# Kernel optimization log

Hardware: AMD Instinct MI355X
Metric: run time of the kernel (lower is better)

## Reference

```python
import jax, jax.numpy as jnp
import numpy as np

NUM_GRAPHS = 256  # B: number of graphs in the ragged batch
EMBED = 256       # input_dim / MHA embed_dim
N_NODES = 200000


def setup_inputs() -> dict:
    key = jax.random.key(0)
    k1, k2, k3, k4, k5, k6 = jax.random.split(key, 6)
    x = jax.random.normal(k1, (N_NODES, EMBED), dtype=jnp.float32)
    in_proj_w = jax.random.normal(k2, (3 * EMBED, EMBED), dtype=jnp.float32) * 0.02
    in_proj_b = jax.random.normal(k3, (3 * EMBED,), dtype=jnp.float32) * 0.02
    out_proj_w = jax.random.normal(k4, (EMBED, EMBED), dtype=jnp.float32) * 0.02
    out_proj_b = jax.random.normal(k5, (EMBED,), dtype=jnp.float32) * 0.02
    batch = jnp.sort(jax.random.randint(k6, (N_NODES,), 0, NUM_GRAPHS)).astype(jnp.int64)
    return {"x": x, "in_proj_w": in_proj_w, "in_proj_b": in_proj_b,
            "out_proj_w": out_proj_w, "out_proj_b": out_proj_b, "batch": batch}


def reference(x, in_proj_w, in_proj_b, out_proj_w, out_proj_b, batch):
    E = x.shape[1]
    # global_mean_pool: per-graph mean of node features -> [B, E]
    sums = jax.ops.segment_sum(x, batch, num_segments=NUM_GRAPHS)
    counts = jax.ops.segment_sum(jnp.ones((x.shape[0],), x.dtype), batch,
                                 num_segments=NUM_GRAPHS)
    g = sums / jnp.maximum(counts, 1.0)[:, None]  # [B, E]
    # MultiheadAttention with a single K/V vector per graph: softmax over S=1
    # is identically 1, so attention output = out_proj(V_proj(g)) for every
    # query node of that graph (Q path contributes nothing).
    Wv = in_proj_w[2 * E:3 * E]
    bv = in_proj_b[2 * E:3 * E]
    v = g @ Wv.T + bv                       # [B, E] value projection
    out_graph = v @ out_proj_w.T + out_proj_b  # [B, E] output projection
    # broadcast back to nodes (torch.cat over per-graph slices)
    return out_graph[batch]                 # [N, E]
```

## Files before the change

### kernel.cpp

```cpp
#include <hip/hip_runtime.h>

#define EMBED   256
#define NGRAPH  256
#define NW      8
#define BLOCK   (NW * 64)

__global__ __launch_bounds__(BLOCK, 1) void fused_kernel(
    const float* __restrict__ x, const int* __restrict__ batch,
    const float* __restrict__ in_w, const float* __restrict__ in_b,
    const float* __restrict__ out_w, const float* __restrict__ out_b,
    float* __restrict__ out, int nNodes) {
  const int g = blockIdx.x;
  const int t = threadIdx.x;
  const int q  = t >> 6;
  const int c4 = t & 63;

  int n0, n1;
  { int a = 0, b = nNodes;
    while (a < b) { int m = (a + b) >> 1; (batch[m] < g) ? (a = m + 1) : (b = m); }
    n0 = a; }
  { int a = n0, b = nNodes;
    while (a < b) { int m = (a + b) >> 1; (batch[m] <= g) ? (a = m + 1) : (b = m); }
    n1 = a; }
  const int cnt = n1 - n0;

  const float4* xp = (const float4*)x + (size_t)n0 * (EMBED / 4) + c4;
  float4 a0 = make_float4(0.f, 0.f, 0.f, 0.f);
  float4 a1 = make_float4(0.f, 0.f, 0.f, 0.f);
  int i = q;
  for (; i + 7 * NW < cnt; i += 8 * NW) {
    float4 v0 = xp[(size_t)(i         ) * (EMBED / 4)];
    float4 v1 = xp[(size_t)(i + 1 * NW) * (EMBED / 4)];
    float4 v2 = xp[(size_t)(i + 2 * NW) * (EMBED / 4)];
    float4 v3 = xp[(size_t)(i + 3 * NW) * (EMBED / 4)];
    float4 v4 = xp[(size_t)(i + 4 * NW) * (EMBED / 4)];
    float4 v5 = xp[(size_t)(i + 5 * NW) * (EMBED / 4)];
    float4 v6 = xp[(size_t)(i + 6 * NW) * (EMBED / 4)];
    float4 v7 = xp[(size_t)(i + 7 * NW) * (EMBED / 4)];
    a0.x += v0.x + v1.x; a0.y += v0.y + v1.y; a0.z += v0.z + v1.z; a0.w += v0.w + v1.w;
    a1.x += v2.x + v3.x; a1.y += v2.y + v3.y; a1.z += v2.z + v3.z; a1.w += v2.w + v3.w;
    a0.x += v4.x + v5.x; a0.y += v4.y + v5.y; a0.z += v4.z + v5.z; a0.w += v4.w + v5.w;
    a1.x += v6.x + v7.x; a1.y += v6.y + v7.y; a1.z += v6.z + v7.z; a1.w += v6.w + v7.w;
  }
  for (; i < cnt; i += NW) {
    float4 v = xp[(size_t)i * (EMBED / 4)];
    a0.x += v.x; a0.y += v.y; a0.z += v.z; a0.w += v.w;
  }
  a0.x += a1.x; a0.y += a1.y; a0.z += a1.z; a0.w += a1.w;

  __shared__ float4 red4[NW][EMBED / 4];
  __shared__ float sg[EMBED];
  __shared__ float sv[EMBED];
  __shared__ float so[EMBED];
  red4[q][c4] = a0;
  __syncthreads();

  const float inv = 1.0f / fmaxf((float)cnt, 1.0f);
  if (t < EMBED) {
    const float* rf = (const float*)red4;
    float s = 0.f;
#pragma unroll
    for (int k = 0; k < NW; ++k) s += rf[k * EMBED + t];
    sg[t] = s * inv;
  }
  __syncthreads();

  if (t < EMBED) {
    float acc = in_b[2 * EMBED + t];
    const float4* wrow = (const float4*)(in_w + (size_t)(2 * EMBED + t) * EMBED);
#pragma unroll 8
    for (int k4 = 0; k4 < EMBED / 4; ++k4) {
      const float4 w = wrow[k4];
      const int k = k4 * 4;
      acc += sg[k] * w.x + sg[k + 1] * w.y + sg[k + 2] * w.z + sg[k + 3] * w.w;
    }
    sv[t] = acc;
  }
  __syncthreads();

  if (t < EMBED) {
    float acc = out_b[t];
    const float4* wrow = (const float4*)(out_w + (size_t)t * EMBED);
#pragma unroll 8
    for (int k4 = 0; k4 < EMBED / 4; ++k4) {
      const float4 w = wrow[k4];
      const int k = k4 * 4;
      acc += sv[k] * w.x + sv[k + 1] * w.y + sv[k + 2] * w.z + sv[k + 3] * w.w;
    }
    so[t] = acc;
  }
  __syncthreads();

  const float4 oval = ((const float4*)so)[c4];
  float4* op = (float4*)out + c4;
  int n = n0 + q;
  for (; n + 3 * NW < n1; n += 4 * NW) {
    op[(size_t)(n         ) * (EMBED / 4)] = oval;
    op[(size_t)(n + 1 * NW) * (EMBED / 4)] = oval;
    op[(size_t)(n + 2 * NW) * (EMBED / 4)] = oval;
    op[(size_t)(n + 3 * NW) * (EMBED / 4)] = oval;
  }
  for (; n < n1; n += NW) {
    op[(size_t)n * (EMBED / 4)] = oval;
  }
}

extern "C" void kernel_launch(void* const* d_in, const int* in_sizes, int n_in,
                              void* d_out, int out_size, void* d_ws, size_t ws_size,
                              hipStream_t stream) {
  const float* x     = (const float*)d_in[0];
  const float* in_w  = (const float*)d_in[1];
  const float* in_b  = (const float*)d_in[2];
  const float* out_w = (const float*)d_in[3];
  const float* out_b = (const float*)d_in[4];
  const int*   batch = (const int*)d_in[5];
  const int nNodes = in_sizes[5];

  fused_kernel<<<NGRAPH, BLOCK, 0, stream>>>(x, batch, in_w, in_b, out_w, out_b,
                                             (float*)d_out, nNodes);
}
```

Measured before the change: 374.8 us.

## Split fused kernel into partial-sum, per-graph projection, and grid-wide broadcast kernels

The single per-graph kernel becomes three. The first splits each graph's node reduction across four blocks and writes partial sums. The second combines the partials and runs the two matvecs per graph. The third broadcasts rows to all nodes with a grid-stride loop, a batch lookup per element and nontemporal stores. The aim is better occupancy and load balance than 256 blocks with one block per CU, where the reduction and the output writes of each graph were serialized. In exchange it adds two kernel launches, round trips through the workspace, and an extra batch read per output float4. If the workspace is too small, partials fall back to being stored in the output buffer.

```diff
diff --git a/kernel.cpp b/kernel.cpp
--- a/kernel.cpp
+++ b/kernel.cpp
@@ -2,16 +2,21 @@
 
 #define EMBED   256
 #define NGRAPH  256
-#define NW      8
-#define BLOCK   (NW * 64)
+#define P       4
+#define BLOCK1  512
+#define NW1     (BLOCK1 / 64)
+#define WPG     (P * NW1)
+#define BLOCK3  256
+#define NB3     2048
 
-__global__ __launch_bounds__(BLOCK, 1) void fused_kernel(
+typedef float f32x4 __attribute__((ext_vector_type(4)));
+
+__global__ __launch_bounds__(BLOCK1, 8) void seg_partial(
     const float* __restrict__ x, const int* __restrict__ batch,
-    const float* __restrict__ in_w, const float* __restrict__ in_b,
-    const float* __restrict__ out_w, const float* __restrict__ out_b,
-    float* __restrict__ out, int nNodes) {
-  const int g = blockIdx.x;
-  const int t = threadIdx.x;
+    float* __restrict__ partial, int nNodes) {
+  const int g  = blockIdx.x >> 2;
+  const int p  = blockIdx.x & (P - 1);
+  const int t  = threadIdx.x;
   const int q  = t >> 6;
   const int c4 = t & 63;
 
@@ -25,83 +30,114 @@
   const int cnt = n1 - n0;
 
   const float4* xp = (const float4*)x + (size_t)n0 * (EMBED / 4) + c4;
+  const int w = p * NW1 + q;
   float4 a0 = make_float4(0.f, 0.f, 0.f, 0.f);
   float4 a1 = make_float4(0.f, 0.f, 0.f, 0.f);
-  int i = q;
-  for (; i + 7 * NW < cnt; i += 8 * NW) {
-    float4 v0 = xp[(size_t)(i         ) * (EMBED / 4)];
-    float4 v1 = xp[(size_t)(i + 1 * NW) * (EMBED / 4)];
-    float4 v2 = xp[(size_t)(i + 2 * NW) * (EMBED / 4)];
-    float4 v3 = xp[(size_t)(i + 3 * NW) * (EMBED / 4)];
-    float4 v4 = xp[(size_t)(i + 4 * NW) * (EMBED / 4)];
-    float4 v5 = xp[(size_t)(i + 5 * NW) * (EMBED / 4)];
-    float4 v6 = xp[(size_t)(i + 6 * NW) * (EMBED / 4)];
-    float4 v7 = xp[(size_t)(i + 7 * NW) * (EMBED / 4)];
+  int i = w;
+  for (; i + 7 * WPG < cnt; i += 8 * WPG) {
+    float4 v0 = xp[(size_t)(i          ) * (EMBED / 4)];
+    float4 v1 = xp[(size_t)(i + 1 * WPG) * (EMBED / 4)];
+    float4 v2 = xp[(size_t)(i + 2 * WPG) * (EMBED / 4)];
+    float4 v3 = xp[(size_t)(i + 3 * WPG) * (EMBED / 4)];
+    float4 v4 = xp[(size_t)(i + 4 * WPG) * (EMBED / 4)];
+    float4 v5 = xp[(size_t)(i + 5 * WPG) * (EMBED / 4)];
+    float4 v6 = xp[(size_t)(i + 6 * WPG) * (EMBED / 4)];
+    float4 v7 = xp[(size_t)(i + 7 * WPG) * (EMBED / 4)];
     a0.x += v0.x + v1.x; a0.y += v0.y + v1.y; a0.z += v0.z + v1.z; a0.w += v0.w + v1.w;
     a1.x += v2.x + v3.x; a1.y += v2.y + v3.y; a1.z += v2.z + v3.z; a1.w += v2.w + v3.w;
     a0.x += v4.x + v5.x; a0.y += v4.y + v5.y; a0.z += v4.z + v5.z; a0.w += v4.w + v5.w;
     a1.x += v6.x + v7.x; a1.y += v6.y + v7.y; a1.z += v6.z + v7.z; a1.w += v6.w + v7.w;
   }
-  for (; i < cnt; i += NW) {
+  for (; i < cnt; i += WPG) {
     float4 v = xp[(size_t)i * (EMBED / 4)];
     a0.x += v.x; a0.y += v.y; a0.z += v.z; a0.w += v.w;
   }
   a0.x += a1.x; a0.y += a1.y; a0.z += a1.z; a0.w += a1.w;
 
-  __shared__ float4 red4[NW][EMBED / 4];
-  __shared__ float sg[EMBED];
-  __shared__ float sv[EMBED];
-  __shared__ float so[EMBED];
+  __shared__ float4 red4[NW1][EMBED / 4];
   red4[q][c4] = a0;
   __syncthreads();
-
-  const float inv = 1.0f / fmaxf((float)cnt, 1.0f);
   if (t < EMBED) {
     const float* rf = (const float*)red4;
     float s = 0.f;
 #pragma unroll
-    for (int k = 0; k < NW; ++k) s += rf[k * EMBED + t];
-    sg[t] = s * inv;
+    for (int k = 0; k < NW1; ++k) s += rf[k * EMBED + t];
+    partial[((size_t)p * NGRAPH + g) * EMBED + t] = s;
   }
+}
+
+__global__ __launch_bounds__(EMBED, 1) void graph_rows(
+    const float* __restrict__ partial, const int* __restrict__ batch,
+    const float* __restrict__ in_w, const float* __restrict__ in_b,
+    const float* __restrict__ out_w, const float* __restrict__ out_b,
+    float* __restrict__ rows, int nNodes) {
+  const int g = blockIdx.x;
+  const int t = threadIdx.x;
+
+  int n0, n1;
+  { int a = 0, b = nNodes;
+    while (a < b) { int m = (a + b) >> 1; (batch[m] < g) ? (a = m + 1) : (b = m); }
+    n0 = a; }
+  { int a = n0, b = nNodes;
+    while (a < b) { int m = (a + b) >> 1; (batch[m] <= g) ? (a = m + 1) : (b = m); }
+    n1 = a; }
+  const float inv = 1.0f / fmaxf((float)(n1 - n0), 1.0f);
+
+  __shared__ float sg[EMBED];
+  __shared__ float sv[EMBED];
+
+  float s = 0.f;
+#pragma unroll
+  for (int p = 0; p < P; ++p) s += partial[((size_t)p * NGRAPH + g) * EMBED + t];
+  sg[t] = s * inv;
   __syncthreads();
 
-  if (t < EMBED) {
-    float acc = in_b[2 * EMBED + t];
-    const float4* wrow = (const float4*)(in_w + (size_t)(2 * EMBED + t) * EMBED);
+  float acc = in_b[2 * EMBED + t];
+  const float4* wrow = (const float4*)(in_w + (size_t)(2 * EMBED + t) * EMBED);
 #pragma unroll 8
-    for (int k4 = 0; k4 < EMBED / 4; ++k4) {
-      const float4 w = wrow[k4];
-      const int k = k4 * 4;
-      acc += sg[k] * w.x + sg[k + 1] * w.y + sg[k + 2] * w.z + sg[k + 3] * w.w;
-    }
-    sv[t] = acc;
+  for (int k4 = 0; k4 < EMBED / 4; ++k4) {
+    const float4 w = wrow[k4];
+    const int k = k4 * 4;
+    acc += sg[k] * w.x + sg[k + 1] * w.y + sg[k + 2] * w.z + sg[k + 3] * w.w;
   }
+  sv[t] = acc;
   __syncthreads();
 
-  if (t < EMBED) {
-    float acc = out_b[t];
-    const float4* wrow = (const float4*)(out_w + (size_t)t * EMBED);
+  float acc2 = out_b[t];
+  const float4* wrow2 = (const float4*)(out_w + (size_t)t * EMBED);
 #pragma unroll 8
-    for (int k4 = 0; k4 < EMBED / 4; ++k4) {
-      const float4 w = wrow[k4];
-      const int k = k4 * 4;
-      acc += sv[k] * w.x + sv[k + 1] * w.y + sv[k + 2] * w.z + sv[k + 3] * w.w;
-    }
-    so[t] = acc;
+  for (int k4 = 0; k4 < EMBED / 4; ++k4) {
+    const float4 w = wrow2[k4];
+    const int k = k4 * 4;
+    acc2 += sv[k] * w.x + sv[k + 1] * w.y + sv[k + 2] * w.z + sv[k + 3] * w.w;
   }
-  __syncthreads();
+  rows[(size_t)g * EMBED + t] = acc2;
+}
 
-  const float4 oval = ((const float4*)so)[c4];
-  float4* op = (float4*)out + c4;
-  int n = n0 + q;
-  for (; n + 3 * NW < n1; n += 4 * NW) {
-    op[(size_t)(n         ) * (EMBED / 4)] = oval;
-    op[(size_t)(n + 1 * NW) * (EMBED / 4)] = oval;
-    op[(size_t)(n + 2 * NW) * (EMBED / 4)] = oval;
-    op[(size_t)(n + 3 * NW) * (EMBED / 4)] = oval;
+__global__ __launch_bounds__(BLOCK3, 8) void bcast(
+    const float4* __restrict__ rows4, const int* __restrict__ batch,
+    float4* __restrict__ out4, long long total) {
+  const long long stride = (long long)gridDim.x * BLOCK3;
+  long long i = (long long)blockIdx.x * BLOCK3 + threadIdx.x;
+  for (; i + 3 * stride < total; i += 4 * stride) {
+    const long long i0 = i, i1 = i + stride, i2 = i + 2 * stride, i3 = i + 3 * stride;
+    const int g0 = batch[(int)(i0 >> 6)];
+    const int g1 = batch[(int)(i1 >> 6)];
+    const int g2 = batch[(int)(i2 >> 6)];
+    const int g3 = batch[(int)(i3 >> 6)];
+    const float4 r0 = rows4[(g0 << 6) + (int)(i0 & 63)];
+    const float4 r1 = rows4[(g1 << 6) + (int)(i1 & 63)];
+    const float4 r2 = rows4[(g2 << 6) + (int)(i2 & 63)];
+    const float4 r3 = rows4[(g3 << 6) + (int)(i3 & 63)];
+    __builtin_nontemporal_store(*(const f32x4*)&r0, (f32x4*)(out4 + i0));
+    __builtin_nontemporal_store(*(const f32x4*)&r1, (f32x4*)(out4 + i1));
+    __builtin_nontemporal_store(*(const f32x4*)&r2, (f32x4*)(out4 + i2));
+    __builtin_nontemporal_store(*(const f32x4*)&r3, (f32x4*)(out4 + i3));
   }
-  for (; n < n1; n += NW) {
-    op[(size_t)n * (EMBED / 4)] = oval;
+  for (; i < total; i += stride) {
+    const int gg = batch[(int)(i >> 6)];
+    const float4 r = rows4[(gg << 6) + (int)(i & 63)];
+    __builtin_nontemporal_store(*(const f32x4*)&r, (f32x4*)(out4 + i));
   }
 }
 
@@ -116,6 +152,21 @@
   const int*   batch = (const int*)d_in[5];
   const int nNodes = in_sizes[5];
 
-  fused_kernel<<<NGRAPH, BLOCK, 0, stream>>>(x, batch, in_w, in_b, out_w, out_b,
-                                             (float*)d_out, nNodes);
+  const size_t needR = (size_t)NGRAPH * EMBED * sizeof(float);
+  const size_t needP = (size_t)P * NGRAPH * EMBED * sizeof(float);
+
+  float* rows = (float*)d_ws;
+  float* partial;
+  if (ws_size >= needR + needP) {
+    partial = rows + (size_t)NGRAPH * EMBED;
+  } else {
+    partial = (float*)d_out;
+  }
+
+  seg_partial<<<NGRAPH * P, BLOCK1, 0, stream>>>(x, batch, partial, nNodes);
+  graph_rows<<<NGRAPH, EMBED, 0, stream>>>(partial, batch, in_w, in_b,
+                                           out_w, out_b, rows, nNodes);
+  const long long total = (long long)nNodes * (EMBED / 4);
+  bcast<<<NB3, BLOCK3, 0, stream>>>((const float4*)rows, batch,
+                                    (float4*)d_out, total);
 }
```

Result: slower. 386.7 us (+3.2%).
